# Kernel optimization log

Measured on AMD Instinct MI355X. Metric: run time of the kernel, lower is better.

Reference implementation:

```python
import jax, jax.numpy as jnp
import numpy as np

N, D, E = 50000, 128, 100000
H1, H2, H3 = 8, 8, 4
NEG_SLOPE = 0.2  # PyG GATv2Conv default negative_slope


def _gatv2_layer(x, src, dst, Wl, Wr, att, b, heads):
    # GATv2Conv(in=D, out=D, heads=heads, concat=False), share_weights=False
    C = Wl.shape[1] // heads
    xl = (x @ Wl).reshape(-1, heads, C)  # source-side transform (x_j)
    xr = (x @ Wr).reshape(-1, heads, C)  # target-side transform (x_i)
    m = jax.nn.leaky_relu(xl[src] + xr[dst], NEG_SLOPE)      # [E,H,C]
    e = jnp.einsum('ehc,hc->eh', m, att)                      # [E,H]
    # segment softmax over incoming edges of each destination node
    emax = jax.ops.segment_max(e, dst, num_segments=N)        # [N,H]
    a = jnp.exp(e - emax[dst])
    denom = jax.ops.segment_sum(a, dst, num_segments=N)       # [N,H] (>0: self-loops)
    a = a / denom[dst]
    out = jax.ops.segment_sum(xl[src] * a[:, :, None], dst, num_segments=N)  # [N,H,C]
    return out.mean(axis=1) + b  # concat=False -> head mean, then bias


def setup_inputs() -> dict:
    key = jax.random.key(0)
    ks = jax.random.split(key, 16)
    x = jax.random.normal(ks[0], (N, D), dtype=jnp.float32)
    src = jax.random.randint(ks[1], (E,), 0, N)
    dst = jax.random.randint(ks[2], (E,), 0, N)
    src = jnp.where(src == dst, (src + 1) % N, src)  # no pre-existing self loops
    edge_index = jnp.stack([src, dst]).astype(jnp.int64)
    s = 1.0 / np.sqrt(D)
    def lin(k, h):
        return jax.random.uniform(k, (D, h * D), jnp.float32, -s, s)
    def attn(k, h):
        return jax.random.uniform(k, (h, D), jnp.float32, -s, s)
    return {
        'x': x, 'edge_index': edge_index,
        'W1l': lin(ks[3], H1), 'W1r': lin(ks[4], H1), 'att1': attn(ks[5], H1), 'b1': jnp.zeros((D,), jnp.float32),
        'W2l': lin(ks[6], H2), 'W2r': lin(ks[7], H2), 'att2': attn(ks[8], H2), 'b2': jnp.zeros((D,), jnp.float32),
        'W3l': lin(ks[9], H3), 'W3r': lin(ks[10], H3), 'att3': attn(ks[11], H3), 'b3': jnp.zeros((D,), jnp.float32),
    }


def reference(x, edge_index, W1l, W1r, att1, b1, W2l, W2r, att2, b2, W3l, W3r, att3, b3):
    # PyG GATv2Conv adds self loops by default
    loops = jnp.arange(N, dtype=edge_index.dtype)
    src = jnp.concatenate([edge_index[0], loops])
    dst = jnp.concatenate([edge_index[1], loops])
    h = x + _gatv2_layer(x, src, dst, W1l, W1r, att1, b1, H1)
    h = jax.nn.elu(h)  # dropout is identity in eval mode
    h = h + _gatv2_layer(h, src, dst, W2l, W2r, att2, b2, H2)
    h = jax.nn.elu(h)
    h = h + _gatv2_layer(h, src, dst, W3l, W3r, att3, b3, H3)
    return h
```

## Files before the change

kernel.cpp:

```cpp
#include <hip/hip_runtime.h>

#define NN 50000
#define DD 128
#define EE 100000
#define ET (EE + NN)

typedef __attribute__((ext_vector_type(4))) float f32x4;
typedef __attribute__((ext_vector_type(2))) float f32x2;
typedef __attribute__((ext_vector_type(8))) short bf16x8;
typedef __attribute__((ext_vector_type(4))) unsigned short u16x4;

static __device__ __forceinline__ unsigned short f2bf(float f) {
  union { float f; unsigned int u; } v; v.f = f;
  unsigned int r = (v.u + 0x7FFFu + ((v.u >> 16) & 1u)) >> 16;
  return (unsigned short)r;
}
static __device__ __forceinline__ float bf2f(unsigned short s) {
  union { unsigned int u; float f; } v; v.u = ((unsigned int)s) << 16;
  return v.f;
}

__global__ void k_count(const int* __restrict__ ei, int* __restrict__ counts) {
  int i = blockIdx.x * blockDim.x + threadIdx.x;
  if (i >= ET) return;
  int dst = (i < EE) ? ei[EE + i] : (i - EE);
  if (dst < 0 || dst >= NN) return;
  atomicAdd(&counts[dst], 1);
}

__global__ __launch_bounds__(1024) void k_scan(const int* __restrict__ counts,
                                               int* __restrict__ offs,
                                               int* __restrict__ cursor) {
  __shared__ int buf[1024];
  const int tid = threadIdx.x;
  int carry = 0;
  for (int base = 0; base < NN; base += 4096) {
    int i0 = base + tid * 4;
    int v[4];
#pragma unroll
    for (int q = 0; q < 4; ++q) { int i = i0 + q; v[q] = (i < NN) ? counts[i] : 0; }
    int s = v[0] + v[1] + v[2] + v[3];
    buf[tid] = s;
    __syncthreads();
    for (int off = 1; off < 1024; off <<= 1) {
      int t = (tid >= off) ? buf[tid - off] : 0;
      __syncthreads();
      buf[tid] += t;
      __syncthreads();
    }
    int excl = carry + buf[tid] - s;
    int tot = buf[1023];
#pragma unroll
    for (int q = 0; q < 4; ++q) {
      int i = i0 + q;
      if (i < NN) { offs[i] = excl; cursor[i] = excl; }
      excl += v[q];
    }
    carry += tot;
    __syncthreads();
  }
  if (tid == 0) offs[NN] = carry;
}

__global__ void k_fill(const int* __restrict__ ei, int* __restrict__ cursor,
                       int* __restrict__ srcs) {
  int i = blockIdx.x * blockDim.x + threadIdx.x;
  if (i >= ET) return;
  int src, dst;
  if (i < EE) { src = ei[i]; dst = ei[EE + i]; }
  else { src = dst = i - EE; }
  if (dst < 0 || dst >= NN) return;
  if (src < 0 || src >= NN) src = dst;
  int pos = atomicAdd(&cursor[dst], 1);
  if (pos >= 0 && pos < ET) srcs[pos] = src;
}

__global__ void k_wT(const float* __restrict__ W, unsigned short* __restrict__ WT, int Nout) {
  int i = blockIdx.x * blockDim.x + threadIdx.x;
  int total = Nout * DD;
  if (i >= total) return;
  int n = i >> 7, k = i & 127;
  WT[i] = f2bf(W[(size_t)k * Nout + n]);
}

__global__ void k_cvt(const float* __restrict__ in, unsigned short* __restrict__ out, int total4) {
  int i = blockIdx.x * blockDim.x + threadIdx.x;
  if (i >= total4) return;
  f32x4 v = *(const f32x4*)(in + (size_t)i * 4);
  u16x4 w;
  w.x = f2bf(v.x); w.y = f2bf(v.y); w.z = f2bf(v.z); w.w = f2bf(v.w);
  *(u16x4*)(out + (size_t)i * 4) = w;
}

__global__ __launch_bounds__(256) void gemm_bt(
    const unsigned short* __restrict__ A, const unsigned short* __restrict__ WT,
    unsigned short* __restrict__ Cl, unsigned short* __restrict__ Cr,
    int M, int Nout, int lgny) {
  const int f = blockIdx.x;
  const int c = f & ((1 << lgny) - 1);
  const int x = f >> lgny;
  const int z = c & 1, y = c >> 1;
  const int m0 = x * 128, n0 = y * 128;
  unsigned short* C = z ? Cr : Cl;
  const unsigned short* BT = WT + (size_t)z * Nout * DD;

  __shared__ unsigned short As[128 * 128];
  __shared__ unsigned short Bs[128 * 128];
  const int tid = threadIdx.x;
  const int wave = tid >> 6, lane = tid & 63;
  const int hi = lane >> 4, lr = lane & 15;

#pragma unroll
  for (int i = 0; i < 8; ++i) {
    int row = i * 16 + wave * 4 + hi;
    int c16 = lr ^ (row & 7);
    const unsigned short* ga = A + (size_t)(m0 + row) * DD + c16 * 8;
    __builtin_amdgcn_global_load_lds((const __attribute__((address_space(1))) void*)ga,
        (__attribute__((address_space(3))) void*)(As + i * 2048 + wave * 512), 16, 0, 0);
    const unsigned short* gb = BT + (size_t)(n0 + row) * DD + c16 * 8;
    __builtin_amdgcn_global_load_lds((const __attribute__((address_space(1))) void*)gb,
        (__attribute__((address_space(3))) void*)(Bs + i * 2048 + wave * 512), 16, 0, 0);
  }
  __syncthreads();

  const int wr = (wave >> 1) * 64, wc = (wave & 1) * 64;
  f32x4 acc[4][4];
#pragma unroll
  for (int i = 0; i < 4; ++i)
#pragma unroll
    for (int j = 0; j < 4; ++j) acc[i][j] = (f32x4){0.f, 0.f, 0.f, 0.f};

#pragma unroll
  for (int k0 = 0; k0 < 128; k0 += 32) {
    const int ck = (k0 >> 3) + hi;
    bf16x8 af[4], bfr[4];
#pragma unroll
    for (int mi = 0; mi < 4; ++mi) {
      int r = wr + mi * 16 + lr;
      af[mi] = *(const bf16x8*)&As[r * 128 + ((ck ^ (r & 7)) << 3)];
    }
#pragma unroll
    for (int ni = 0; ni < 4; ++ni) {
      int cc = wc + ni * 16 + lr;
      bfr[ni] = *(const bf16x8*)&Bs[cc * 128 + ((ck ^ (cc & 7)) << 3)];
    }
#pragma unroll
    for (int mi = 0; mi < 4; ++mi)
#pragma unroll
      for (int ni = 0; ni < 4; ++ni)
        acc[mi][ni] = __builtin_amdgcn_mfma_f32_16x16x32_bf16(af[mi], bfr[ni], acc[mi][ni], 0, 0, 0);
  }

#pragma unroll
  for (int mi = 0; mi < 4; ++mi) {
#pragma unroll
    for (int ni = 0; ni < 4; ++ni) {
      int col = n0 + wc + ni * 16 + lr;
#pragma unroll
      for (int j = 0; j < 4; ++j) {
        int row = m0 + wr + mi * 16 + (hi << 2) + j;
        if (row < M) C[(size_t)row * Nout + col] = f2bf(acc[mi][ni][j]);
      }
    }
  }
}

template <int H>
__global__ __launch_bounds__(256) void gat_agg(
    const unsigned short* __restrict__ xl, const unsigned short* __restrict__ xr,
    const int* __restrict__ offs, const int* __restrict__ srcs,
    const float* __restrict__ att, const float* __restrict__ bias,
    const float* __restrict__ resid, float* __restrict__ out,
    unsigned short* __restrict__ hbf, int do_elu) {
  const int wave = threadIdx.x >> 6, lane = threadIdx.x & 63;
  const int n = blockIdx.x * 4 + wave;
  if (n >= NN) return;
  const int c0 = lane << 1;

  float xr0[H], xr1[H], a0[H], a1[H];
  float acc0[H], acc1[H], mx[H], dn[H];
#pragma unroll
  for (int h = 0; h < H; ++h) {
    unsigned int u = *(const unsigned int*)(xr + ((size_t)n * H + h) * DD + c0);
    xr0[h] = bf2f((unsigned short)(u & 0xFFFFu));
    xr1[h] = bf2f((unsigned short)(u >> 16));
    a0[h] = att[h * DD + c0];
    a1[h] = att[h * DD + c0 + 1];
    acc0[h] = 0.f; acc1[h] = 0.f; mx[h] = -1e30f; dn[h] = 0.f;
  }

  const int e0 = offs[n], e1 = offs[n + 1];
  for (int j = e0; j < e1; ++j) {
    int s = srcs[j];
#pragma unroll
    for (int h = 0; h < H; ++h) {
      unsigned int u = *(const unsigned int*)(xl + ((size_t)s * H + h) * DD + c0);
      float x0 = bf2f((unsigned short)(u & 0xFFFFu));
      float x1 = bf2f((unsigned short)(u >> 16));
      float z0 = x0 + xr0[h]; z0 = (z0 > 0.f) ? z0 : 0.2f * z0;
      float z1 = x1 + xr1[h]; z1 = (z1 > 0.f) ? z1 : 0.2f * z1;
      float p = z0 * a0[h] + z1 * a1[h];
#pragma unroll
      for (int m = 1; m < 64; m <<= 1) p += __shfl_xor(p, m, 64);
      float mnew = fmaxf(mx[h], p);
      float sc = __expf(mx[h] - mnew);
      float w = __expf(p - mnew);
      acc0[h] = acc0[h] * sc + w * x0;
      acc1[h] = acc1[h] * sc + w * x1;
      dn[h] = dn[h] * sc + w;
      mx[h] = mnew;
    }
  }

  float s0 = 0.f, s1 = 0.f;
#pragma unroll
  for (int h = 0; h < H; ++h) {
    float inv = 1.f / dn[h];
    s0 += acc0[h] * inv;
    s1 += acc1[h] * inv;
  }
  const float invH = 1.f / (float)H;
  float o0 = s0 * invH + bias[c0] + resid[(size_t)n * DD + c0];
  float o1 = s1 * invH + bias[c0 + 1] + resid[(size_t)n * DD + c0 + 1];
  if (do_elu) {
    o0 = (o0 > 0.f) ? o0 : expm1f(o0);
    o1 = (o1 > 0.f) ? o1 : expm1f(o1);
  }
  f32x2 o; o.x = o0; o.y = o1;
  *(f32x2*)(out + (size_t)n * DD + c0) = o;
  if (hbf) {
    unsigned int pk = (unsigned int)f2bf(o0) | ((unsigned int)f2bf(o1) << 16);
    *(unsigned int*)(hbf + (size_t)n * DD + c0) = pk;
  }
}

extern "C" void kernel_launch(void* const* d_in, const int* in_sizes, int n_in,
                              void* d_out, int out_size, void* d_ws, size_t ws_size,
                              hipStream_t stream) {
  const float* x = (const float*)d_in[0];
  const int* ei = (const int*)d_in[1];
  const float* W1l = (const float*)d_in[2];
  const float* W1r = (const float*)d_in[3];
  const float* att1 = (const float*)d_in[4];
  const float* b1 = (const float*)d_in[5];
  const float* W2l = (const float*)d_in[6];
  const float* W2r = (const float*)d_in[7];
  const float* att2 = (const float*)d_in[8];
  const float* b2 = (const float*)d_in[9];
  const float* W3l = (const float*)d_in[10];
  const float* W3r = (const float*)d_in[11];
  const float* att3 = (const float*)d_in[12];
  const float* b3 = (const float*)d_in[13];
  float* out = (float*)d_out;

  char* p = (char*)d_ws;
  auto carve = [&](size_t bytes) {
    char* r = p;
    p += (bytes + 255) & ~(size_t)255;
    return r;
  };
  unsigned short* xl = (unsigned short*)carve((size_t)NN * 1024 * 2);
  unsigned short* xr = (unsigned short*)carve((size_t)NN * 1024 * 2);
  unsigned short* abf = (unsigned short*)carve((size_t)NN * DD * 2);
  unsigned short* wt1 = (unsigned short*)carve((size_t)2 * 1024 * DD * 2);
  unsigned short* wt2 = (unsigned short*)carve((size_t)2 * 1024 * DD * 2);
  unsigned short* wt3 = (unsigned short*)carve((size_t)2 * 512 * DD * 2);
  int* counts = (int*)carve((size_t)NN * 4);
  int* offs = (int*)carve(((size_t)NN + 1) * 4);
  int* cursor = (int*)carve((size_t)NN * 4);
  int* srcs = (int*)carve((size_t)ET * 4);
  size_t needed = (size_t)(p - (char*)d_ws);
  if (needed > ws_size) return;

  hipMemsetAsync(counts, 0, (size_t)NN * 4, stream);
  k_count<<<(ET + 255) / 256, 256, 0, stream>>>(ei, counts);
  k_scan<<<1, 1024, 0, stream>>>(counts, offs, cursor);
  k_fill<<<(ET + 255) / 256, 256, 0, stream>>>(ei, cursor, srcs);

  k_wT<<<(1024 * DD + 255) / 256, 256, 0, stream>>>(W1l, wt1, 1024);
  k_wT<<<(1024 * DD + 255) / 256, 256, 0, stream>>>(W1r, wt1 + (size_t)1024 * DD, 1024);
  k_wT<<<(1024 * DD + 255) / 256, 256, 0, stream>>>(W2l, wt2, 1024);
  k_wT<<<(1024 * DD + 255) / 256, 256, 0, stream>>>(W2r, wt2 + (size_t)1024 * DD, 1024);
  k_wT<<<(512 * DD + 255) / 256, 256, 0, stream>>>(W3l, wt3, 512);
  k_wT<<<(512 * DD + 255) / 256, 256, 0, stream>>>(W3r, wt3 + (size_t)512 * DD, 512);

  k_cvt<<<((NN * DD / 4) + 255) / 256, 256, 0, stream>>>(x, abf, NN * DD / 4);

  const int gx = (NN + 127) / 128;
  gemm_bt<<<gx * 16, 256, 0, stream>>>(abf, wt1, xl, xr, NN, 1024, 4);
  gat_agg<8><<<(NN + 3) / 4, 256, 0, stream>>>(xl, xr, offs, srcs, att1, b1, x, out, abf, 1);
  gemm_bt<<<gx * 16, 256, 0, stream>>>(abf, wt2, xl, xr, NN, 1024, 4);
  gat_agg<8><<<(NN + 3) / 4, 256, 0, stream>>>(xl, xr, offs, srcs, att2, b2, out, out, abf, 1);
  gemm_bt<<<gx * 8, 256, 0, stream>>>(abf, wt3, xl, xr, NN, 512, 3);
  gat_agg<4><<<(NN + 3) / 4, 256, 0, stream>>>(xl, xr, offs, srcs, att3, b3, out, out, nullptr, 0);
}
```

Before: 544.4 us.

## Remap GATv2 aggregation lanes to contiguous per-head channel chunks with prefetch

Reworks the aggregation kernel so each lane owns 2H contiguous channels within a single head. The per-edge dot-product reduction then needs only log2(64/H) shuffles instead of a full 64-lane reduction per head. It adds software prefetching of the next source row, pre-scales attention by log2(e) so it can use exp2, and uses a lazy max-rescale threshold to skip most rescales of the online softmax. The head mean is done by a final cross-lane shuffle. The cost is more registers per lane, which may reduce occupancy, plus a slight numerical difference from the deferred rescaling.

```diff
diff --git a/kernel.cpp b/kernel.cpp
--- a/kernel.cpp
+++ b/kernel.cpp
@@ -9,15 +9,18 @@
 typedef __attribute__((ext_vector_type(2))) float f32x2;
 typedef __attribute__((ext_vector_type(8))) short bf16x8;
 typedef __attribute__((ext_vector_type(4))) unsigned short u16x4;
+typedef __attribute__((ext_vector_type(4))) unsigned int u32x4;
 
 static __device__ __forceinline__ unsigned short f2bf(float f) {
   union { float f; unsigned int u; } v; v.f = f;
   unsigned int r = (v.u + 0x7FFFu + ((v.u >> 16) & 1u)) >> 16;
   return (unsigned short)r;
 }
-static __device__ __forceinline__ float bf2f(unsigned short s) {
-  union { unsigned int u; float f; } v; v.u = ((unsigned int)s) << 16;
-  return v.f;
+static __device__ __forceinline__ float bflo(unsigned int u) {
+  union { unsigned int u; float f; } v; v.u = u << 16; return v.f;
+}
+static __device__ __forceinline__ float bfhi(unsigned int u) {
+  union { unsigned int u; float f; } v; v.u = u & 0xffff0000u; return v.f;
 }
 
 __global__ void k_count(const int* __restrict__ ei, int* __restrict__ counts) {
@@ -90,6 +93,12 @@
   u16x4 w;
   w.x = f2bf(v.x); w.y = f2bf(v.y); w.z = f2bf(v.z); w.w = f2bf(v.w);
   *(u16x4*)(out + (size_t)i * 4) = w;
+}
+
+__global__ void k_atts(const float* __restrict__ a, float* __restrict__ o, int total) {
+  int i = blockIdx.x * blockDim.x + threadIdx.x;
+  if (i >= total) return;
+  o[i] = a[i] * 1.4426950408889634f;
 }
 
 __global__ __launch_bounds__(256) void gemm_bt(
@@ -166,71 +175,117 @@
 }
 
 template <int H>
-__global__ __launch_bounds__(256) void gat_agg(
+__global__ __launch_bounds__(256) void gat_agg2(
     const unsigned short* __restrict__ xl, const unsigned short* __restrict__ xr,
     const int* __restrict__ offs, const int* __restrict__ srcs,
-    const float* __restrict__ att, const float* __restrict__ bias,
+    const float* __restrict__ att_s,
+    const float* __restrict__ bias,
     const float* __restrict__ resid, float* __restrict__ out,
     unsigned short* __restrict__ hbf, int do_elu) {
+  constexpr int LPH = 64 / H;
+  constexpr int CPL = 2 * H;
+  constexpr int NW = H;
+  constexpr int ROW = H * DD;
   const int wave = threadIdx.x >> 6, lane = threadIdx.x & 63;
   const int n = blockIdx.x * 4 + wave;
   if (n >= NN) return;
-  const int c0 = lane << 1;
-
-  float xr0[H], xr1[H], a0[H], a1[H];
-  float acc0[H], acc1[H], mx[H], dn[H];
-#pragma unroll
-  for (int h = 0; h < H; ++h) {
-    unsigned int u = *(const unsigned int*)(xr + ((size_t)n * H + h) * DD + c0);
-    xr0[h] = bf2f((unsigned short)(u & 0xFFFFu));
-    xr1[h] = bf2f((unsigned short)(u >> 16));
-    a0[h] = att[h * DD + c0];
-    a1[h] = att[h * DD + c0 + 1];
-    acc0[h] = 0.f; acc1[h] = 0.f; mx[h] = -1e30f; dn[h] = 0.f;
-  }
+  const int cb = lane * CPL;
+
+  float xrv[CPL], av[CPL];
+  {
+    const unsigned int* q = (const unsigned int*)(xr + (size_t)n * ROW + cb);
+#pragma unroll
+    for (int w = 0; w < NW; ++w) {
+      unsigned int u = q[w];
+      xrv[2 * w] = bflo(u);
+      xrv[2 * w + 1] = bfhi(u);
+    }
+#pragma unroll
+    for (int c = 0; c < CPL; ++c) av[c] = att_s[cb + c];
+  }
+
+  float acc[CPL];
+#pragma unroll
+  for (int c = 0; c < CPL; ++c) acc[c] = 0.f;
+  float mx = -1e30f, dn = 0.f;
 
   const int e0 = offs[n], e1 = offs[n + 1];
+  unsigned int cur[NW], nxt[NW];
+  {
+    int s = srcs[e0];
+    const unsigned int* q = (const unsigned int*)(xl + (size_t)s * ROW + cb);
+#pragma unroll
+    for (int w = 0; w < NW; ++w) cur[w] = q[w];
+  }
   for (int j = e0; j < e1; ++j) {
-    int s = srcs[j];
-#pragma unroll
-    for (int h = 0; h < H; ++h) {
-      unsigned int u = *(const unsigned int*)(xl + ((size_t)s * H + h) * DD + c0);
-      float x0 = bf2f((unsigned short)(u & 0xFFFFu));
-      float x1 = bf2f((unsigned short)(u >> 16));
-      float z0 = x0 + xr0[h]; z0 = (z0 > 0.f) ? z0 : 0.2f * z0;
-      float z1 = x1 + xr1[h]; z1 = (z1 > 0.f) ? z1 : 0.2f * z1;
-      float p = z0 * a0[h] + z1 * a1[h];
-#pragma unroll
-      for (int m = 1; m < 64; m <<= 1) p += __shfl_xor(p, m, 64);
-      float mnew = fmaxf(mx[h], p);
-      float sc = __expf(mx[h] - mnew);
-      float w = __expf(p - mnew);
-      acc0[h] = acc0[h] * sc + w * x0;
-      acc1[h] = acc1[h] * sc + w * x1;
-      dn[h] = dn[h] * sc + w;
-      mx[h] = mnew;
-    }
-  }
-
-  float s0 = 0.f, s1 = 0.f;
-#pragma unroll
-  for (int h = 0; h < H; ++h) {
-    float inv = 1.f / dn[h];
-    s0 += acc0[h] * inv;
-    s1 += acc1[h] * inv;
-  }
-  const float invH = 1.f / (float)H;
-  float o0 = s0 * invH + bias[c0] + resid[(size_t)n * DD + c0];
-  float o1 = s1 * invH + bias[c0 + 1] + resid[(size_t)n * DD + c0 + 1];
-  if (do_elu) {
-    o0 = (o0 > 0.f) ? o0 : expm1f(o0);
-    o1 = (o1 > 0.f) ? o1 : expm1f(o1);
-  }
-  f32x2 o; o.x = o0; o.y = o1;
-  *(f32x2*)(out + (size_t)n * DD + c0) = o;
-  if (hbf) {
-    unsigned int pk = (unsigned int)f2bf(o0) | ((unsigned int)f2bf(o1) << 16);
-    *(unsigned int*)(hbf + (size_t)n * DD + c0) = pk;
+    if (j + 1 < e1) {
+      int s2 = srcs[j + 1];
+      const unsigned int* q = (const unsigned int*)(xl + (size_t)s2 * ROW + cb);
+#pragma unroll
+      for (int w = 0; w < NW; ++w) nxt[w] = q[w];
+    }
+    float xv[CPL];
+#pragma unroll
+    for (int w = 0; w < NW; ++w) {
+      xv[2 * w] = bflo(cur[w]);
+      xv[2 * w + 1] = bfhi(cur[w]);
+    }
+    float p = 0.f;
+#pragma unroll
+    for (int c = 0; c < CPL; ++c) {
+      float z = xv[c] + xrv[c];
+      z = fmaxf(z, 0.2f * z);
+      p = fmaf(z, av[c], p);
+    }
+#pragma unroll
+    for (int m = 1; m < LPH; m <<= 1) p += __shfl_xor(p, m, 64);
+    if (__any(p > mx + 11.5f)) {
+      float mnew = fmaxf(mx, p);
+      float sc = __builtin_amdgcn_exp2f(mx - mnew);
+      dn *= sc;
+#pragma unroll
+      for (int c = 0; c < CPL; ++c) acc[c] *= sc;
+      mx = mnew;
+    }
+    float wt = __builtin_amdgcn_exp2f(p - mx);
+    dn += wt;
+#pragma unroll
+    for (int c = 0; c < CPL; ++c) acc[c] = fmaf(wt, xv[c], acc[c]);
+#pragma unroll
+    for (int w = 0; w < NW; ++w) cur[w] = nxt[w];
+  }
+
+  float r[CPL];
+  const float inv = (1.f / (float)H) / dn;
+#pragma unroll
+  for (int c = 0; c < CPL; ++c) r[c] = acc[c] * inv;
+#pragma unroll
+  for (int m = LPH; m < 64; m <<= 1)
+#pragma unroll
+    for (int c = 0; c < CPL; ++c) r[c] += __shfl_xor(r[c], m, 64);
+
+  if (lane < LPH) {
+    float o[CPL];
+#pragma unroll
+    for (int c = 0; c < CPL; ++c) {
+      o[c] = r[c] + bias[cb + c] + resid[(size_t)n * DD + cb + c];
+      if (do_elu) o[c] = (o[c] > 0.f) ? o[c] : expm1f(o[c]);
+    }
+#pragma unroll
+    for (int c = 0; c < CPL; c += 4) {
+      f32x4 v; v.x = o[c]; v.y = o[c + 1]; v.z = o[c + 2]; v.w = o[c + 3];
+      *(f32x4*)(out + (size_t)n * DD + cb + c) = v;
+    }
+    if (hbf) {
+#pragma unroll
+      for (int c = 0; c < CPL; c += 8) {
+        u32x4 pk;
+#pragma unroll
+        for (int q = 0; q < 4; ++q)
+          pk[q] = (unsigned int)f2bf(o[c + 2 * q]) | ((unsigned int)f2bf(o[c + 2 * q + 1]) << 16);
+        *(u32x4*)(hbf + (size_t)n * DD + cb + c) = pk;
+      }
+    }
   }
 }
 
@@ -265,6 +320,9 @@
   unsigned short* wt1 = (unsigned short*)carve((size_t)2 * 1024 * DD * 2);
   unsigned short* wt2 = (unsigned short*)carve((size_t)2 * 1024 * DD * 2);
   unsigned short* wt3 = (unsigned short*)carve((size_t)2 * 512 * DD * 2);
+  float* as1 = (float*)carve((size_t)8 * DD * 4);
+  float* as2 = (float*)carve((size_t)8 * DD * 4);
+  float* as3 = (float*)carve((size_t)4 * DD * 4);
   int* counts = (int*)carve((size_t)NN * 4);
   int* offs = (int*)carve(((size_t)NN + 1) * 4);
   int* cursor = (int*)carve((size_t)NN * 4);
@@ -283,14 +341,17 @@
   k_wT<<<(1024 * DD + 255) / 256, 256, 0, stream>>>(W2r, wt2 + (size_t)1024 * DD, 1024);
   k_wT<<<(512 * DD + 255) / 256, 256, 0, stream>>>(W3l, wt3, 512);
   k_wT<<<(512 * DD + 255) / 256, 256, 0, stream>>>(W3r, wt3 + (size_t)512 * DD, 512);
+  k_atts<<<4, 256, 0, stream>>>(att1, as1, 8 * DD);
+  k_atts<<<4, 256, 0, stream>>>(att2, as2, 8 * DD);
+  k_atts<<<2, 256, 0, stream>>>(att3, as3, 4 * DD);
 
   k_cvt<<<((NN * DD / 4) + 255) / 256, 256, 0, stream>>>(x, abf, NN * DD / 4);
 
   const int gx = (NN + 127) / 128;
   gemm_bt<<<gx * 16, 256, 0, stream>>>(abf, wt1, xl, xr, NN, 1024, 4);
-  gat_agg<8><<<(NN + 3) / 4, 256, 0, stream>>>(xl, xr, offs, srcs, att1, b1, x, out, abf, 1);
+  gat_agg2<8><<<(NN + 3) / 4, 256, 0, stream>>>(xl, xr, offs, srcs, as1, b1, x, out, abf, 1);
   gemm_bt<<<gx * 16, 256, 0, stream>>>(abf, wt2, xl, xr, NN, 1024, 4);
-  gat_agg<8><<<(NN + 3) / 4, 256, 0, stream>>>(xl, xr, offs, srcs, att2, b2, out, out, abf, 1);
+  gat_agg2<8><<<(NN + 3) / 4, 256, 0, stream>>>(xl, xr, offs, srcs, as2, b2, out, out, abf, 1);
   gemm_bt<<<gx * 8, 256, 0, stream>>>(abf, wt3, xl, xr, NN, 512, 3);
-  gat_agg<4><<<(NN + 3) / 4, 256, 0, stream>>>(xl, xr, offs, srcs, att3, b3, out, out, nullptr, 0);
-}
+  gat_agg2<4><<<(NN + 3) / 4, 256, 0, stream>>>(xl, xr, offs, srcs, as3, b3, out, out, nullptr, 0);
+}
```

Result: no change. 544.0 us (-0.1%).
